# Kernel optimization log

Measured on AMD Instinct MI355X. Metric: run time of the kernel, lower is better.

The kernel has to match this reference:

```python
import jax, jax.numpy as jnp
import numpy as np
import math

B, N, D = 8, 4096, 1024
H = 8          # num_heads
NC = 2         # n_classes


def setup_inputs() -> dict:
    key = jax.random.key(0)
    ks = jax.random.split(key, 12)
    s = 1.0 / math.sqrt(D)
    return {
        "inputs": jax.random.normal(ks[0], (B, N, D), jnp.float32),
        # enc: Linear(D, 1) + Sigmoid
        "W_enc": jax.random.normal(ks[1], (1, D), jnp.float32) * s,
        "b_enc": jnp.zeros((1,), jnp.float32),
        "cls_token": jax.random.normal(ks[2], (1, 1, D), jnp.float32) * s,
        # depthwise Conv2d(D, D, 3, padding=1, groups=D)
        "conv_w": jax.random.normal(ks[3], (D, 1, 3, 3), jnp.float32) * 0.1,
        "conv_b": jnp.zeros((D,), jnp.float32),
        # MAB projections (torch Linear weight layout [out, in])
        "Wq": jax.random.normal(ks[4], (D, D), jnp.float32) * s,
        "bq": jnp.zeros((D,), jnp.float32),
        "Wk": jax.random.normal(ks[5], (D, D), jnp.float32) * s,
        "bk": jnp.zeros((D,), jnp.float32),
        "Wv": jax.random.normal(ks[6], (D, D), jnp.float32) * s,
        "bv": jnp.zeros((D,), jnp.float32),
        "Wo": jax.random.normal(ks[7], (D, D), jnp.float32) * s,
        "bo": jnp.zeros((D,), jnp.float32),
        # final classifier Linear(D, NC)
        "Wfc": jax.random.normal(ks[8], (NC, D), jnp.float32) * s,
        "bfc": jnp.zeros((NC,), jnp.float32),
    }


def reference(inputs, W_enc, b_enc, cls_token, conv_w, conv_b,
              Wq, bq, Wk, bk, Wv, bv, Wo, bo, Wfc, bfc):
    b, n, d = inputs.shape
    # ---- recalib(option='max', k=1): top-1 instance per bag as query ----
    a1 = jax.nn.sigmoid(inputs @ W_enc.T + b_enc)[..., 0]            # [B, N]
    idx = jnp.argmax(a1, axis=1)                                      # [B]
    Q = jnp.take_along_axis(inputs, idx[:, None, None], axis=1)       # [B, 1, D]
    # ---- shift_feature ----
    inputs = jax.nn.relu(inputs - Q)
    # ---- pad to square grid, prepend cls token ----
    _H = int(np.ceil(np.sqrt(n)))
    add = _H * _H - n
    x = jnp.concatenate([inputs, inputs[:, :add, :]], axis=1)         # [B, _H*_H, D]
    cls = jnp.broadcast_to(cls_token, (b, 1, d))
    x = jnp.concatenate([cls, x], axis=1)                             # [B, S, D]
    cls_tok, feat = x[:, 0], x[:, 1:]
    # ---- depthwise conv residual on the 2D grid ----
    cnn = feat.transpose(0, 2, 1).reshape(b, d, _H, _H)               # [B, C, H, W]
    conv = jax.lax.conv_general_dilated(
        cnn, conv_w, window_strides=(1, 1), padding='SAME',
        dimension_numbers=('NCHW', 'OIHW', 'NCHW'),
        feature_group_count=d) + conv_b[None, :, None, None]
    cnn = conv + cnn
    xf = cnn.reshape(b, d, _H * _H).transpose(0, 2, 1)
    x = jnp.concatenate([cls_tok[:, None, :], xf], axis=1)            # [B, S, D]
    # ---- MAB(Q, x): manual multi-head attention ----
    Qp = Q @ Wq.T + bq                                                # [B, 1, D]
    K = x @ Wk.T + bk                                                 # [B, S, D]
    V = x @ Wv.T + bv
    dh = d // H
    qh = Qp.reshape(b, 1, H, dh).transpose(0, 2, 1, 3)                # [B, H, 1, dh]
    kh = K.reshape(b, -1, H, dh).transpose(0, 2, 1, 3)                # [B, H, S, dh]
    vh = V.reshape(b, -1, H, dh).transpose(0, 2, 1, 3)
    # NOTE: original scales by sqrt(dim_V), not sqrt(d_head)
    logits = jnp.einsum('bhqd,bhkd->bhqk', qh, kh) / jnp.asarray(math.sqrt(d), jnp.float32)
    A = jax.nn.softmax(logits, axis=-1)
    oh = qh + jnp.einsum('bhqk,bhkd->bhqd', A, vh)                    # residual inside heads
    O = oh.transpose(0, 2, 1, 3).reshape(b, 1, d)                     # [B, 1, D]
    O = O + jax.nn.relu(O @ Wo.T + bo)
    bag = O[:, 0]                                                     # [B, D]
    out = bag @ Wfc.T + bfc                                           # [B, NC]
    return out
```

## Files before the change

### kernel.cpp

```cpp
#include <hip/hip_runtime.h>
#include <hip/hip_bf16.h>


#define NTOK 4096
#define DD 1024

#define FO_ARG 0
#define FO_CWT 4160
#define FO_QP  13376
#define FO_W   21568
#define FO_MS  87232
#define FO_YP  95424
#define FO_Y   4289728
#define FO_O1  4355264
#define FO_O2  4363456
#define FO_XF  8388608
#define FO_PL  41943040

#define LSTRIDE 101

__global__ void k_init(const float* __restrict__ convw, float* __restrict__ cwT,
                       unsigned long long* __restrict__ argbest) {
  int gid = blockIdx.x * 256 + threadIdx.x;
  if (gid < 8) argbest[gid] = 0ull;
  if (gid < 9216) {
    int d = gid / 9, p = gid - d * 9;
    cwT[p * DD + d] = convw[gid];
  }
}

__global__ void k_argmax1(const float* __restrict__ inp, const float* __restrict__ Wenc,
                          const float* __restrict__ benc, unsigned long long* __restrict__ argbest) {
  __shared__ unsigned long long lb[4];
  int wave = threadIdx.x >> 6, lane = threadIdx.x & 63;
  int b = blockIdx.x >> 8;
  int r0 = ((blockIdx.x & 255) << 4) + (wave << 2);
  const float4* base = (const float4*)(inp + ((size_t)b * NTOK + r0) * DD);
  const float4* wp = (const float4*)Wenc;
  float s0 = 0.f, s1 = 0.f, s2 = 0.f, s3 = 0.f;
#pragma unroll
  for (int k = 0; k < 4; ++k) {
    int off = lane + (k << 6);
    float4 w4 = wp[off];
    float4 a0 = base[off];
    float4 a1 = base[256 + off];
    float4 a2 = base[512 + off];
    float4 a3 = base[768 + off];
    s0 = fmaf(w4.x, a0.x, s0); s0 = fmaf(w4.y, a0.y, s0); s0 = fmaf(w4.z, a0.z, s0); s0 = fmaf(w4.w, a0.w, s0);
    s1 = fmaf(w4.x, a1.x, s1); s1 = fmaf(w4.y, a1.y, s1); s1 = fmaf(w4.z, a1.z, s1); s1 = fmaf(w4.w, a1.w, s1);
    s2 = fmaf(w4.x, a2.x, s2); s2 = fmaf(w4.y, a2.y, s2); s2 = fmaf(w4.z, a2.z, s2); s2 = fmaf(w4.w, a2.w, s2);
    s3 = fmaf(w4.x, a3.x, s3); s3 = fmaf(w4.y, a3.y, s3); s3 = fmaf(w4.z, a3.z, s3); s3 = fmaf(w4.w, a3.w, s3);
  }
#pragma unroll
  for (int mk = 32; mk >= 1; mk >>= 1) {
    s0 += __shfl_xor(s0, mk); s1 += __shfl_xor(s1, mk);
    s2 += __shfl_xor(s2, mk); s3 += __shfl_xor(s3, mk);
  }
  if (lane == 0) {
    float be = benc[0];
    float v[4] = {s0 + be, s1 + be, s2 + be, s3 + be};
    unsigned long long bst = 0ull;
#pragma unroll
    for (int i = 0; i < 4; ++i) {
      unsigned u = __float_as_uint(v[i]);
      u = (u & 0x80000000u) ? ~u : (u | 0x80000000u);
      unsigned long long p = ((unsigned long long)u << 32) |
                             (unsigned long long)(0xFFFFFFFFu - (unsigned)(r0 + i));
      bst = bst > p ? bst : p;
    }
    lb[wave] = bst;
  }
  __syncthreads();
  if (threadIdx.x == 0) {
    unsigned long long m = lb[0];
#pragma unroll
    for (int i = 1; i < 4; ++i) m = m > lb[i] ? m : lb[i];
    atomicMax(&argbest[b], m);
  }
}

__global__ void k_qp(const float* __restrict__ inp, const float* __restrict__ Wq,
                     const float* __restrict__ bq, const unsigned long long* __restrict__ argbest,
                     float* __restrict__ Qp) {
  int wave = threadIdx.x >> 6, lane = threadIdx.x & 63;
  int b = blockIdx.x >> 8;
  int i = ((blockIdx.x & 255) << 2) + wave;
  unsigned idx = 0xFFFFFFFFu - (unsigned)(argbest[b] & 0xFFFFFFFFull);
  const float4* qr = (const float4*)(inp + ((size_t)b * NTOK + idx) * DD);
  const float4* wr = (const float4*)(Wq + (size_t)i * DD);
  float s = 0.f;
#pragma unroll
  for (int k = 0; k < 4; ++k) {
    float4 a = wr[lane + (k << 6)], x = qr[lane + (k << 6)];
    s = fmaf(a.x, x.x, s); s = fmaf(a.y, x.y, s);
    s = fmaf(a.z, x.z, s); s = fmaf(a.w, x.w, s);
  }
  for (int m = 32; m > 0; m >>= 1) s += __shfl_xor(s, m);
  if (lane == 0) Qp[b * DD + i] = s + bq[i];
}

__global__ void k_w(const float* __restrict__ Wk, const float* __restrict__ Qp,
                    float* __restrict__ wbuf) {
  __shared__ float qs[1024];
  __shared__ float sred[2048];
  const int tid = threadIdx.x;
  const int h = blockIdx.x >> 5, jb = blockIdx.x & 31;
  {
    int b = tid >> 5, i4 = tid & 31;
    ((float4*)qs)[b * 32 + i4] = ((const float4*)Qp)[b * 256 + (h << 5) + i4];
  }
  __syncthreads();
  const int jl = tid & 31, ig = tid >> 5;
  const float* wkp = Wk + (size_t)((h << 7) + (ig << 4)) * DD + (jb << 5) + jl;
  float acc[8];
#pragma unroll
  for (int b = 0; b < 8; ++b) acc[b] = 0.f;
#pragma unroll
  for (int ii = 0; ii < 16; ++ii) {
    float wv = wkp[(size_t)ii * DD];
    int i = (ig << 4) + ii;
#pragma unroll
    for (int b = 0; b < 8; ++b) acc[b] = fmaf(qs[(b << 7) + i], wv, acc[b]);
  }
#pragma unroll
  for (int b = 0; b < 8; ++b) sred[ig * 256 + (b << 5) + jl] = acc[b];
  __syncthreads();
  {
    int b = tid >> 5, j2 = tid & 31;
    float s = 0.f;
#pragma unroll
    for (int g = 0; g < 8; ++g) s += sred[g * 256 + (b << 5) + j2];
    wbuf[(size_t)((b << 3) + h) * DD + (jb << 5) + j2] = s;
  }
}

__global__ __launch_bounds__(512, 4) void k_logits(
    const float* __restrict__ inp, const float* __restrict__ convb,
    const float* __restrict__ cwT, const float* __restrict__ wbuf,
    const unsigned long long* __restrict__ argbest,
    float* __restrict__ plog, float* __restrict__ xf) {
  __shared__ float4 sred4[2048];
  const int tid = threadIdx.x, bx = blockIdx.x;
  const int b = bx >> 10, tile = (bx >> 4) & 63, cidx = bx & 15;
  const int R0 = (tile >> 3) << 3, C0 = (tile & 7) << 3;
  const unsigned idxq = 0xFFFFFFFFu - (unsigned)(argbest[b] & 0xFFFFFFFFull);
  const float* inpb = inp + (size_t)b * NTOK * DD;
  const float* qrow = inpb + (size_t)idxq * DD;
  const int gg = tid & 15, ts = tid >> 4;
  const int jg = tid >> 5, rq = (tid >> 3) & 3, ca = tid & 7;
  const int r0a = rq << 1;
  const int jc = cidx << 6;

  float acc[2][8];
#pragma unroll
  for (int i = 0; i < 2; ++i)
#pragma unroll
    for (int h = 0; h < 8; ++h) acc[i][h] = 0.f;
  float4 xs0, xs1;

  {
    const int js = jc + (gg << 2);
    float4 qv = *(const float4*)(qrow + js);
    for (int t = ts; t < 100; t += 32) {
      int tr = t / 10, tc = t - tr * 10;
      int gr = R0 - 1 + tr, gc = C0 - 1 + tc;
      float4 v = make_float4(0.f, 0.f, 0.f, 0.f);
      if (gr >= 0 && gr < 64 && gc >= 0 && gc < 64) {
        float4 rv = *(const float4*)(inpb + (size_t)((gr << 6) + gc) * DD + js);
        v.x = fmaxf(rv.x - qv.x, 0.f); v.y = fmaxf(rv.y - qv.y, 0.f);
        v.z = fmaxf(rv.z - qv.z, 0.f); v.w = fmaxf(rv.w - qv.w, 0.f);
      }
      sred4[gg * LSTRIDE + t] = v;
    }
  }
  __syncthreads();
  {
    const int j4 = jc + (jg << 2);
    float4 cwr[9];
#pragma unroll
    for (int p = 0; p < 9; ++p) cwr[p] = *(const float4*)(cwT + p * DD + j4);
    float4 cb4 = *(const float4*)(convb + j4);
    const float4* fb = sred4 + jg * LSTRIDE;
    float4 x0 = cb4, x1 = cb4;
    {
      float4 rw[4][3];
#pragma unroll
      for (int rr = 0; rr < 4; ++rr)
#pragma unroll
        for (int dc = 0; dc < 3; ++dc)
          rw[rr][dc] = fb[(r0a + rr) * 10 + ca + dc];
#pragma unroll
      for (int dr = 0; dr < 3; ++dr)
#pragma unroll
        for (int dc = 0; dc < 3; ++dc) {
          float4 w = cwr[dr * 3 + dc];
          float4 f0 = rw[dr][dc], f1 = rw[dr + 1][dc];
          x0.x = fmaf(w.x, f0.x, x0.x); x0.y = fmaf(w.y, f0.y, x0.y);
          x0.z = fmaf(w.z, f0.z, x0.z); x0.w = fmaf(w.w, f0.w, x0.w);
          x1.x = fmaf(w.x, f1.x, x1.x); x1.y = fmaf(w.y, f1.y, x1.y);
          x1.z = fmaf(w.z, f1.z, x1.z); x1.w = fmaf(w.w, f1.w, x1.w);
        }
      x0.x += rw[1][1].x; x0.y += rw[1][1].y; x0.z += rw[1][1].z; x0.w += rw[1][1].w;
      x1.x += rw[2][1].x; x1.y += rw[2][1].y; x1.z += rw[2][1].z; x1.w += rw[2][1].w;
    }
    xs0 = x0; xs1 = x1;
#pragma unroll
    for (int h = 0; h < 8; ++h) {
      float4 whv = *(const float4*)(wbuf + (size_t)(b * 8 + h) * DD + j4);
      float a0 = acc[0][h], a1 = acc[1][h];
      a0 = fmaf(whv.x, x0.x, a0); a0 = fmaf(whv.y, x0.y, a0);
      a0 = fmaf(whv.z, x0.z, a0); a0 = fmaf(whv.w, x0.w, a0);
      a1 = fmaf(whv.x, x1.x, a1); a1 = fmaf(whv.y, x1.y, a1);
      a1 = fmaf(whv.z, x1.z, a1); a1 = fmaf(whv.w, x1.w, a1);
      acc[0][h] = a0; acc[1][h] = a1;
    }
  }
  __syncthreads();
  float* red = (float*)sred4;
#pragma unroll
  for (int it = 0; it < 2; ++it)
#pragma unroll
    for (int h = 0; h < 8; ++h)
      red[jg * 512 + ((r0a + it) * 8 + ca) * 8 + h] = acc[it][h];
  __syncthreads();
  {
    float s = 0.f;
#pragma unroll
    for (int g = 0; g < 16; ++g) s += red[g * 512 + tid];
    plog[(size_t)bx * 512 + tid] = s;
  }
  __syncthreads();
  float4* ldsx = sred4;
  {
    const int tk0 = (r0a << 3) + ca;
    ldsx[tk0 * 17 + jg] = xs0;
    ldsx[(tk0 + 8) * 17 + jg] = xs1;
  }
  __syncthreads();
  {
    float* xfb = xf + (size_t)((b << 6) + tile) * (64 * DD) + jc;
#pragma unroll
    for (int it = 0; it < 2; ++it) {
      int idx = (it << 9) + tid;
      int tk = idx >> 4, q = idx & 15;
      float4 v = ldsx[tk * 17 + q];
      *(float4*)(xfb + (size_t)tk * DD + (q << 2)) = v;
    }
  }
}

__global__ __launch_bounds__(512, 8) void k_ysum(
    const float* __restrict__ plog, const float* __restrict__ xf,
    float2* __restrict__ msbuf, float* __restrict__ ypart) {
  __shared__ float atile[512];
  const int tid = threadIdx.x, bt = blockIdx.x;
  {
    const float* pp = plog + (size_t)bt * 16 * 512;
    float s = 0.f;
#pragma unroll
    for (int c = 0; c < 16; ++c) s += pp[c * 512 + tid];
    atile[tid] = s * 0.03125f;
  }
  __syncthreads();
  {
    const int w = tid >> 6, l = tid & 63;
    float v = atile[l * 8 + w];
    float mx = v;
#pragma unroll
    for (int mk = 32; mk >= 1; mk >>= 1) mx = fmaxf(mx, __shfl_xor(mx, mk));
    float e = __expf(v - mx);
    float Ss = e;
#pragma unroll
    for (int mk = 32; mk >= 1; mk >>= 1) Ss += __shfl_xor(Ss, mk);
    __syncthreads();
    atile[l * 8 + w] = e;
    if (l == 0) {
      int b = bt >> 6, tile = bt & 63;
      msbuf[((b << 3) + w) * 64 + tile] = make_float2(mx, Ss);
    }
  }
  __syncthreads();
  const float* xbase = xf + (size_t)bt * (64 * DD) + (tid << 1);
  float2 acc[8];
#pragma unroll
  for (int h = 0; h < 8; ++h) acc[h] = make_float2(0.f, 0.f);
#pragma unroll 4
  for (int t = 0; t < 64; ++t) {
    float2 v = *(const float2*)(xbase + (size_t)t * DD);
    float4 aA = *(const float4*)&atile[t * 8];
    float4 aB = *(const float4*)&atile[t * 8 + 4];
    acc[0].x = fmaf(aA.x, v.x, acc[0].x); acc[0].y = fmaf(aA.x, v.y, acc[0].y);
    acc[1].x = fmaf(aA.y, v.x, acc[1].x); acc[1].y = fmaf(aA.y, v.y, acc[1].y);
    acc[2].x = fmaf(aA.z, v.x, acc[2].x); acc[2].y = fmaf(aA.z, v.y, acc[2].y);
    acc[3].x = fmaf(aA.w, v.x, acc[3].x); acc[3].y = fmaf(aA.w, v.y, acc[3].y);
    acc[4].x = fmaf(aB.x, v.x, acc[4].x); acc[4].y = fmaf(aB.x, v.y, acc[4].y);
    acc[5].x = fmaf(aB.y, v.x, acc[5].x); acc[5].y = fmaf(aB.y, v.y, acc[5].y);
    acc[6].x = fmaf(aB.z, v.x, acc[6].x); acc[6].y = fmaf(aB.z, v.y, acc[6].y);
    acc[7].x = fmaf(aB.w, v.x, acc[7].x); acc[7].y = fmaf(aB.w, v.y, acc[7].y);
  }
  const int b = bt >> 6, tile = bt & 63;
#pragma unroll
  for (int h = 0; h < 8; ++h)
    *(float2*)(ypart + ((size_t)((b * 8 + h) * 64 + tile)) * DD + (tid << 1)) = acc[h];
}

__global__ void k_comb(const float2* __restrict__ msbuf, const float* __restrict__ wbuf,
                       const float* __restrict__ cls, const float* __restrict__ ypart,
                       float* __restrict__ ybuf) {
  __shared__ float redl[256];
  __shared__ float wgt[64];
  __shared__ float wclss;
  __shared__ float4 sacc[256];
  int tid = threadIdx.x;
  int bh = blockIdx.x >> 3, cs = blockIdx.x & 7;
  {
    float4 a = ((const float4*)(wbuf + (size_t)bh * DD))[tid];
    float4 c = ((const float4*)cls)[tid];
    redl[tid] = a.x * c.x + a.y * c.y + a.z * c.z + a.w * c.w;
  }
  __syncthreads();
  for (int s = 128; s > 0; s >>= 1) { if (tid < s) redl[tid] += redl[tid + s]; __syncthreads(); }
  float l0 = redl[0] * 0.03125f;
  if (tid < 64) {
    float2 ms = msbuf[bh * 64 + tid];
    float m = ms.x, S = ms.y;
    float M = m;
#pragma unroll
    for (int mk = 32; mk >= 1; mk >>= 1) M = fmaxf(M, __shfl_xor(M, mk));
    M = fmaxf(M, l0);
    float w = __expf(m - M);
    float z = S * w;
#pragma unroll
    for (int mk = 32; mk >= 1; mk >>= 1) z += __shfl_xor(z, mk);
    float ec = __expf(l0 - M);
    float Z = z + ec;
    wgt[tid] = w / Z;
    if (tid == 0) wclss = ec / Z;
  }
  __syncthreads();
  int ch4 = (cs << 5) + (tid & 31);
  int tg = tid >> 5;
  const float* yp = ypart + (size_t)bh * 64 * DD + (ch4 << 2);
  float4 acc = make_float4(0.f, 0.f, 0.f, 0.f);
#pragma unroll
  for (int tt = 0; tt < 8; ++tt) {
    int t = tg * 8 + tt;
    float w = wgt[t];
    float4 v = *(const float4*)(yp + (size_t)t * DD);
    acc.x = fmaf(w, v.x, acc.x); acc.y = fmaf(w, v.y, acc.y);
    acc.z = fmaf(w, v.z, acc.z); acc.w = fmaf(w, v.w, acc.w);
  }
  sacc[tg * 32 + (tid & 31)] = acc;
  __syncthreads();
  if (tid < 32) {
    int c4 = (cs << 5) + tid;
    float4 s = sacc[tid];
#pragma unroll
    for (int g = 1; g < 8; ++g) {
      float4 v = sacc[g * 32 + tid];
      s.x += v.x; s.y += v.y; s.z += v.z; s.w += v.w;
    }
    float wc = wclss;
    float4 cv = *(const float4*)(cls + (c4 << 2));
    s.x = fmaf(wc, cv.x, s.x); s.y = fmaf(wc, cv.y, s.y);
    s.z = fmaf(wc, cv.z, s.z); s.w = fmaf(wc, cv.w, s.w);
    *(float4*)(ybuf + (size_t)bh * DD + (c4 << 2)) = s;
  }
}

__global__ void k_o1(const float* __restrict__ Wv, const float* __restrict__ bv,
                     const float* __restrict__ Qp, const float* __restrict__ ybuf,
                     float* __restrict__ O1) {
  int wave = threadIdx.x >> 6, lane = threadIdx.x & 63;
  int b = blockIdx.x >> 8;
  int i = ((blockIdx.x & 255) << 2) + wave;
  int h = i >> 7;
  const float4* wr = (const float4*)(Wv + (size_t)i * DD);
  const float4* yr = (const float4*)(ybuf + (size_t)(b * 8 + h) * DD);
  float s = 0.f;
#pragma unroll
  for (int k = 0; k < 4; ++k) {
    float4 a = wr[lane + (k << 6)], x = yr[lane + (k << 6)];
    s = fmaf(a.x, x.x, s); s = fmaf(a.y, x.y, s);
    s = fmaf(a.z, x.z, s); s = fmaf(a.w, x.w, s);
  }
  for (int m = 32; m > 0; m >>= 1) s += __shfl_xor(s, m);
  if (lane == 0) O1[b * DD + i] = Qp[b * DD + i] + bv[i] + s;
}

__global__ void k_o2(const float* __restrict__ Wo, const float* __restrict__ bo,
                     const float* __restrict__ O1, float* __restrict__ O2) {
  int wave = threadIdx.x >> 6, lane = threadIdx.x & 63;
  int b = blockIdx.x >> 8;
  int i = ((blockIdx.x & 255) << 2) + wave;
  const float4* wr = (const float4*)(Wo + (size_t)i * DD);
  const float4* xr = (const float4*)(O1 + (size_t)b * DD);
  float s = 0.f;
#pragma unroll
  for (int k = 0; k < 4; ++k) {
    float4 a = wr[lane + (k << 6)], x = xr[lane + (k << 6)];
    s = fmaf(a.x, x.x, s); s = fmaf(a.y, x.y, s);
    s = fmaf(a.z, x.z, s); s = fmaf(a.w, x.w, s);
  }
  for (int m = 32; m > 0; m >>= 1) s += __shfl_xor(s, m);
  if (lane == 0) O2[b * DD + i] = O1[b * DD + i] + fmaxf(s + bo[i], 0.f);
}

__global__ void k_out(const float* __restrict__ Wfc, const float* __restrict__ bfc,
                      const float* __restrict__ O2, float* __restrict__ out) {
  int wave = threadIdx.x >> 6, lane = threadIdx.x & 63;
  for (int p = wave; p < 16; p += 4) {
    int b = p >> 1, cc = p & 1;
    const float4* o = (const float4*)(O2 + (size_t)b * DD);
    const float4* wr = (const float4*)(Wfc + (size_t)cc * DD);
    float s = 0.f;
#pragma unroll
    for (int k = 0; k < 4; ++k) {
      float4 a = o[lane + (k << 6)], x = wr[lane + (k << 6)];
      s = fmaf(a.x, x.x, s); s = fmaf(a.y, x.y, s);
      s = fmaf(a.z, x.z, s); s = fmaf(a.w, x.w, s);
    }
    for (int m = 32; m > 0; m >>= 1) s += __shfl_xor(s, m);
    if (lane == 0) out[p] = s + bfc[cc];
  }
}

extern "C" void kernel_launch(void* const* d_in, const int* in_sizes, int n_in,
                              void* d_out, int out_size, void* d_ws, size_t ws_size,
                              hipStream_t stream) {
  const float* inp   = (const float*)d_in[0];
  const float* Wenc  = (const float*)d_in[1];
  const float* benc  = (const float*)d_in[2];
  const float* cls   = (const float*)d_in[3];
  const float* convw = (const float*)d_in[4];
  const float* convb = (const float*)d_in[5];
  const float* Wq    = (const float*)d_in[6];
  const float* bq    = (const float*)d_in[7];
  const float* Wk    = (const float*)d_in[8];
  const float* bv    = (const float*)d_in[11];
  const float* Wv    = (const float*)d_in[10];
  const float* Wo    = (const float*)d_in[12];
  const float* bo    = (const float*)d_in[13];
  const float* Wfc   = (const float*)d_in[14];
  const float* bfc   = (const float*)d_in[15];
  float* out = (float*)d_out;
  float* W = (float*)d_ws;
  unsigned long long* argbest = (unsigned long long*)(W + FO_ARG);
  float* cwT   = W + FO_CWT;
  float* Qp    = W + FO_QP;
  float* wbuf  = W + FO_W;
  float2* msbuf = (float2*)(W + FO_MS);
  float* ypart = W + FO_YP;
  float* plog  = W + FO_PL;
  float* xf    = W + FO_XF;
  float* ybuf  = W + FO_Y;
  float* O1    = W + FO_O1;
  float* O2    = W + FO_O2;

  hipLaunchKernelGGL(k_init,    dim3(36),   dim3(256), 0, stream, convw, cwT, argbest);
  hipLaunchKernelGGL(k_argmax1, dim3(2048), dim3(256), 0, stream, inp, Wenc, benc, argbest);
  hipLaunchKernelGGL(k_qp,      dim3(2048), dim3(256), 0, stream, inp, Wq, bq, argbest, Qp);
  hipLaunchKernelGGL(k_w,       dim3(256),  dim3(256), 0, stream, Wk, Qp, wbuf);
  hipLaunchKernelGGL(k_logits,  dim3(8192), dim3(512), 0, stream, inp, convb, cwT, wbuf, argbest, plog, xf);
  hipLaunchKernelGGL(k_ysum,    dim3(512),  dim3(512), 0, stream, plog, xf, msbuf, ypart);
  hipLaunchKernelGGL(k_comb,    dim3(512),  dim3(256), 0, stream, msbuf, wbuf, cls, ypart, ybuf);
  hipLaunchKernelGGL(k_o1,      dim3(2048), dim3(256), 0, stream, Wv, bv, Qp, ybuf, O1);
  hipLaunchKernelGGL(k_o2,      dim3(2048), dim3(256), 0, stream, Wo, bo, O1, O2);
  hipLaunchKernelGGL(k_out,     dim3(1),    dim3(256), 0, stream, Wfc, bfc, O2, out);
}
```

Baseline: 339.8 us.

## Fuse conv/logits and softmax-weighted sum into one kernel keeping features in registers

Merges k_logits and k_ysum into k_fuse. Each block now handles a whole 8x8 tile across all 1024 channels, looping over 16 channel chunks and holding the conv outputs in registers (32 float4). This removes the global round trip of xf and plog, about 128MB of writes and reads. The cost is only 512 blocks with heavy register pressure, launch bounds cut to 2 per SIMD, possible spills, and cross-lane shuffle reductions for the weighted sums.

After: 488.8 us. 1.44x slower.

```diff
diff --git a/kernel.cpp b/kernel.cpp
--- a/kernel.cpp
+++ b/kernel.cpp
@@ -14,8 +14,6 @@
 #define FO_Y   4289728
 #define FO_O1  4355264
 #define FO_O2  4363456
-#define FO_XF  8388608
-#define FO_PL  41943040
 
 #define LSTRIDE 101
 
@@ -134,14 +132,15 @@
   }
 }
 
-__global__ __launch_bounds__(512, 4) void k_logits(
+__global__ __launch_bounds__(512, 2) void k_fuse(
     const float* __restrict__ inp, const float* __restrict__ convb,
     const float* __restrict__ cwT, const float* __restrict__ wbuf,
     const unsigned long long* __restrict__ argbest,
-    float* __restrict__ plog, float* __restrict__ xf) {
+    float2* __restrict__ msbuf, float* __restrict__ ypart) {
   __shared__ float4 sred4[2048];
+  __shared__ float atile[512];
   const int tid = threadIdx.x, bx = blockIdx.x;
-  const int b = bx >> 10, tile = (bx >> 4) & 63, cidx = bx & 15;
+  const int b = bx >> 6, tile = bx & 63;
   const int R0 = (tile >> 3) << 3, C0 = (tile & 7) << 3;
   const unsigned idxq = 0xFFFFFFFFu - (unsigned)(argbest[b] & 0xFFFFFFFFull);
   const float* inpb = inp + (size_t)b * NTOK * DD;
@@ -149,70 +148,75 @@
   const int gg = tid & 15, ts = tid >> 4;
   const int jg = tid >> 5, rq = (tid >> 3) & 3, ca = tid & 7;
   const int r0a = rq << 1;
-  const int jc = cidx << 6;
+  const int tk0 = (r0a << 3) + ca;
 
   float acc[2][8];
 #pragma unroll
   for (int i = 0; i < 2; ++i)
 #pragma unroll
     for (int h = 0; h < 8; ++h) acc[i][h] = 0.f;
-  float4 xs0, xs1;
-
-  {
-    const int js = jc + (gg << 2);
-    float4 qv = *(const float4*)(qrow + js);
-    for (int t = ts; t < 100; t += 32) {
-      int tr = t / 10, tc = t - tr * 10;
-      int gr = R0 - 1 + tr, gc = C0 - 1 + tc;
-      float4 v = make_float4(0.f, 0.f, 0.f, 0.f);
-      if (gr >= 0 && gr < 64 && gc >= 0 && gc < 64) {
-        float4 rv = *(const float4*)(inpb + (size_t)((gr << 6) + gc) * DD + js);
-        v.x = fmaxf(rv.x - qv.x, 0.f); v.y = fmaxf(rv.y - qv.y, 0.f);
-        v.z = fmaxf(rv.z - qv.z, 0.f); v.w = fmaxf(rv.w - qv.w, 0.f);
+  float4 xsA[16], xsB[16];
+
+#pragma unroll
+  for (int cidx = 0; cidx < 16; ++cidx) {
+    const int jc = cidx << 6;
+    if (cidx) __syncthreads();
+    {
+      const int js = jc + (gg << 2);
+      float4 qv = *(const float4*)(qrow + js);
+      for (int t = ts; t < 100; t += 32) {
+        int tr = t / 10, tc = t - tr * 10;
+        int gr = R0 - 1 + tr, gc = C0 - 1 + tc;
+        float4 v = make_float4(0.f, 0.f, 0.f, 0.f);
+        if (gr >= 0 && gr < 64 && gc >= 0 && gc < 64) {
+          float4 rv = *(const float4*)(inpb + (size_t)((gr << 6) + gc) * DD + js);
+          v.x = fmaxf(rv.x - qv.x, 0.f); v.y = fmaxf(rv.y - qv.y, 0.f);
+          v.z = fmaxf(rv.z - qv.z, 0.f); v.w = fmaxf(rv.w - qv.w, 0.f);
+        }
+        sred4[gg * LSTRIDE + t] = v;
       }
-      sred4[gg * LSTRIDE + t] = v;
-    }
-  }
-  __syncthreads();
-  {
-    const int j4 = jc + (jg << 2);
-    float4 cwr[9];
-#pragma unroll
-    for (int p = 0; p < 9; ++p) cwr[p] = *(const float4*)(cwT + p * DD + j4);
-    float4 cb4 = *(const float4*)(convb + j4);
-    const float4* fb = sred4 + jg * LSTRIDE;
-    float4 x0 = cb4, x1 = cb4;
+    }
+    __syncthreads();
     {
-      float4 rw[4][3];
-#pragma unroll
-      for (int rr = 0; rr < 4; ++rr)
-#pragma unroll
-        for (int dc = 0; dc < 3; ++dc)
-          rw[rr][dc] = fb[(r0a + rr) * 10 + ca + dc];
-#pragma unroll
-      for (int dr = 0; dr < 3; ++dr)
-#pragma unroll
-        for (int dc = 0; dc < 3; ++dc) {
-          float4 w = cwr[dr * 3 + dc];
-          float4 f0 = rw[dr][dc], f1 = rw[dr + 1][dc];
-          x0.x = fmaf(w.x, f0.x, x0.x); x0.y = fmaf(w.y, f0.y, x0.y);
-          x0.z = fmaf(w.z, f0.z, x0.z); x0.w = fmaf(w.w, f0.w, x0.w);
-          x1.x = fmaf(w.x, f1.x, x1.x); x1.y = fmaf(w.y, f1.y, x1.y);
-          x1.z = fmaf(w.z, f1.z, x1.z); x1.w = fmaf(w.w, f1.w, x1.w);
-        }
-      x0.x += rw[1][1].x; x0.y += rw[1][1].y; x0.z += rw[1][1].z; x0.w += rw[1][1].w;
-      x1.x += rw[2][1].x; x1.y += rw[2][1].y; x1.z += rw[2][1].z; x1.w += rw[2][1].w;
-    }
-    xs0 = x0; xs1 = x1;
-#pragma unroll
-    for (int h = 0; h < 8; ++h) {
-      float4 whv = *(const float4*)(wbuf + (size_t)(b * 8 + h) * DD + j4);
-      float a0 = acc[0][h], a1 = acc[1][h];
-      a0 = fmaf(whv.x, x0.x, a0); a0 = fmaf(whv.y, x0.y, a0);
-      a0 = fmaf(whv.z, x0.z, a0); a0 = fmaf(whv.w, x0.w, a0);
-      a1 = fmaf(whv.x, x1.x, a1); a1 = fmaf(whv.y, x1.y, a1);
-      a1 = fmaf(whv.z, x1.z, a1); a1 = fmaf(whv.w, x1.w, a1);
-      acc[0][h] = a0; acc[1][h] = a1;
+      const int j4 = jc + (jg << 2);
+      float4 cwr[9];
+#pragma unroll
+      for (int p = 0; p < 9; ++p) cwr[p] = *(const float4*)(cwT + p * DD + j4);
+      float4 cb4 = *(const float4*)(convb + j4);
+      const float4* fb = sred4 + jg * LSTRIDE;
+      float4 x0 = cb4, x1 = cb4;
+      {
+        float4 rw[4][3];
+#pragma unroll
+        for (int rr = 0; rr < 4; ++rr)
+#pragma unroll
+          for (int dc = 0; dc < 3; ++dc)
+            rw[rr][dc] = fb[(r0a + rr) * 10 + ca + dc];
+#pragma unroll
+        for (int dr = 0; dr < 3; ++dr)
+#pragma unroll
+          for (int dc = 0; dc < 3; ++dc) {
+            float4 w = cwr[dr * 3 + dc];
+            float4 f0 = rw[dr][dc], f1 = rw[dr + 1][dc];
+            x0.x = fmaf(w.x, f0.x, x0.x); x0.y = fmaf(w.y, f0.y, x0.y);
+            x0.z = fmaf(w.z, f0.z, x0.z); x0.w = fmaf(w.w, f0.w, x0.w);
+            x1.x = fmaf(w.x, f1.x, x1.x); x1.y = fmaf(w.y, f1.y, x1.y);
+            x1.z = fmaf(w.z, f1.z, x1.z); x1.w = fmaf(w.w, f1.w, x1.w);
+          }
+        x0.x += rw[1][1].x; x0.y += rw[1][1].y; x0.z += rw[1][1].z; x0.w += rw[1][1].w;
+        x1.x += rw[2][1].x; x1.y += rw[2][1].y; x1.z += rw[2][1].z; x1.w += rw[2][1].w;
+      }
+      xsA[cidx] = x0; xsB[cidx] = x1;
+#pragma unroll
+      for (int h = 0; h < 8; ++h) {
+        float4 whv = *(const float4*)(wbuf + (size_t)(b * 8 + h) * DD + j4);
+        float a0 = acc[0][h], a1 = acc[1][h];
+        a0 = fmaf(whv.x, x0.x, a0); a0 = fmaf(whv.y, x0.y, a0);
+        a0 = fmaf(whv.z, x0.z, a0); a0 = fmaf(whv.w, x0.w, a0);
+        a1 = fmaf(whv.x, x1.x, a1); a1 = fmaf(whv.y, x1.y, a1);
+        a1 = fmaf(whv.z, x1.z, a1); a1 = fmaf(whv.w, x1.w, a1);
+        acc[0][h] = a0; acc[1][h] = a1;
+      }
     }
   }
   __syncthreads();
@@ -227,38 +231,6 @@
     float s = 0.f;
 #pragma unroll
     for (int g = 0; g < 16; ++g) s += red[g * 512 + tid];
-    plog[(size_t)bx * 512 + tid] = s;
-  }
-  __syncthreads();
-  float4* ldsx = sred4;
-  {
-    const int tk0 = (r0a << 3) + ca;
-    ldsx[tk0 * 17 + jg] = xs0;
-    ldsx[(tk0 + 8) * 17 + jg] = xs1;
-  }
-  __syncthreads();
-  {
-    float* xfb = xf + (size_t)((b << 6) + tile) * (64 * DD) + jc;
-#pragma unroll
-    for (int it = 0; it < 2; ++it) {
-      int idx = (it << 9) + tid;
-      int tk = idx >> 4, q = idx & 15;
-      float4 v = ldsx[tk * 17 + q];
-      *(float4*)(xfb + (size_t)tk * DD + (q << 2)) = v;
-    }
-  }
-}
-
-__global__ __launch_bounds__(512, 8) void k_ysum(
-    const float* __restrict__ plog, const float* __restrict__ xf,
-    float2* __restrict__ msbuf, float* __restrict__ ypart) {
-  __shared__ float atile[512];
-  const int tid = threadIdx.x, bt = blockIdx.x;
-  {
-    const float* pp = plog + (size_t)bt * 16 * 512;
-    float s = 0.f;
-#pragma unroll
-    for (int c = 0; c < 16; ++c) s += pp[c * 512 + tid];
     atile[tid] = s * 0.03125f;
   }
   __syncthreads();
@@ -274,34 +246,57 @@
     for (int mk = 32; mk >= 1; mk >>= 1) Ss += __shfl_xor(Ss, mk);
     __syncthreads();
     atile[l * 8 + w] = e;
-    if (l == 0) {
-      int b = bt >> 6, tile = bt & 63;
-      msbuf[((b << 3) + w) * 64 + tile] = make_float2(mx, Ss);
-    }
-  }
-  __syncthreads();
-  const float* xbase = xf + (size_t)bt * (64 * DD) + (tid << 1);
-  float2 acc[8];
-#pragma unroll
-  for (int h = 0; h < 8; ++h) acc[h] = make_float2(0.f, 0.f);
-#pragma unroll 4
-  for (int t = 0; t < 64; ++t) {
-    float2 v = *(const float2*)(xbase + (size_t)t * DD);
-    float4 aA = *(const float4*)&atile[t * 8];
-    float4 aB = *(const float4*)&atile[t * 8 + 4];
-    acc[0].x = fmaf(aA.x, v.x, acc[0].x); acc[0].y = fmaf(aA.x, v.y, acc[0].y);
-    acc[1].x = fmaf(aA.y, v.x, acc[1].x); acc[1].y = fmaf(aA.y, v.y, acc[1].y);
-    acc[2].x = fmaf(aA.z, v.x, acc[2].x); acc[2].y = fmaf(aA.z, v.y, acc[2].y);
-    acc[3].x = fmaf(aA.w, v.x, acc[3].x); acc[3].y = fmaf(aA.w, v.y, acc[3].y);
-    acc[4].x = fmaf(aB.x, v.x, acc[4].x); acc[4].y = fmaf(aB.x, v.y, acc[4].y);
-    acc[5].x = fmaf(aB.y, v.x, acc[5].x); acc[5].y = fmaf(aB.y, v.y, acc[5].y);
-    acc[6].x = fmaf(aB.z, v.x, acc[6].x); acc[6].y = fmaf(aB.z, v.y, acc[6].y);
-    acc[7].x = fmaf(aB.w, v.x, acc[7].x); acc[7].y = fmaf(aB.w, v.y, acc[7].y);
-  }
-  const int b = bt >> 6, tile = bt & 63;
-#pragma unroll
-  for (int h = 0; h < 8; ++h)
-    *(float2*)(ypart + ((size_t)((b * 8 + h) * 64 + tile)) * DD + (tid << 1)) = acc[h];
+    if (l == 0) msbuf[((b << 3) + w) * 64 + tile] = make_float2(mx, Ss);
+  }
+  __syncthreads();
+  float* yout = (float*)sred4;
+  const float4 aA = *(const float4*)&atile[tk0 * 8];
+  const float4 aB = *(const float4*)&atile[tk0 * 8 + 4];
+  const float4 cA = *(const float4*)&atile[(tk0 + 8) * 8];
+  const float4 cB = *(const float4*)&atile[(tk0 + 8) * 8 + 4];
+#pragma unroll
+  for (int cidx = 0; cidx < 16; ++cidx) {
+    float4 x0 = xsA[cidx], x1 = xsB[cidx];
+    float4 y[8];
+    y[0].x = fmaf(aA.x, x0.x, cA.x * x1.x); y[0].y = fmaf(aA.x, x0.y, cA.x * x1.y);
+    y[0].z = fmaf(aA.x, x0.z, cA.x * x1.z); y[0].w = fmaf(aA.x, x0.w, cA.x * x1.w);
+    y[1].x = fmaf(aA.y, x0.x, cA.y * x1.x); y[1].y = fmaf(aA.y, x0.y, cA.y * x1.y);
+    y[1].z = fmaf(aA.y, x0.z, cA.y * x1.z); y[1].w = fmaf(aA.y, x0.w, cA.y * x1.w);
+    y[2].x = fmaf(aA.z, x0.x, cA.z * x1.x); y[2].y = fmaf(aA.z, x0.y, cA.z * x1.y);
+    y[2].z = fmaf(aA.z, x0.z, cA.z * x1.z); y[2].w = fmaf(aA.z, x0.w, cA.z * x1.w);
+    y[3].x = fmaf(aA.w, x0.x, cA.w * x1.x); y[3].y = fmaf(aA.w, x0.y, cA.w * x1.y);
+    y[3].z = fmaf(aA.w, x0.z, cA.w * x1.z); y[3].w = fmaf(aA.w, x0.w, cA.w * x1.w);
+    y[4].x = fmaf(aB.x, x0.x, cB.x * x1.x); y[4].y = fmaf(aB.x, x0.y, cB.x * x1.y);
+    y[4].z = fmaf(aB.x, x0.z, cB.x * x1.z); y[4].w = fmaf(aB.x, x0.w, cB.x * x1.w);
+    y[5].x = fmaf(aB.y, x0.x, cB.y * x1.x); y[5].y = fmaf(aB.y, x0.y, cB.y * x1.y);
+    y[5].z = fmaf(aB.y, x0.z, cB.y * x1.z); y[5].w = fmaf(aB.y, x0.w, cB.y * x1.w);
+    y[6].x = fmaf(aB.z, x0.x, cB.z * x1.x); y[6].y = fmaf(aB.z, x0.y, cB.z * x1.y);
+    y[6].z = fmaf(aB.z, x0.z, cB.z * x1.z); y[6].w = fmaf(aB.z, x0.w, cB.z * x1.w);
+    y[7].x = fmaf(aB.w, x0.x, cB.w * x1.x); y[7].y = fmaf(aB.w, x0.y, cB.w * x1.y);
+    y[7].z = fmaf(aB.w, x0.z, cB.w * x1.z); y[7].w = fmaf(aB.w, x0.w, cB.w * x1.w);
+#pragma unroll
+    for (int mk = 16; mk >= 1; mk >>= 1)
+#pragma unroll
+      for (int h = 0; h < 8; ++h) {
+        y[h].x += __shfl_xor(y[h].x, mk);
+        y[h].y += __shfl_xor(y[h].y, mk);
+        y[h].z += __shfl_xor(y[h].z, mk);
+        y[h].w += __shfl_xor(y[h].w, mk);
+      }
+    if ((tid & 31) == 0) {
+#pragma unroll
+      for (int h = 0; h < 8; ++h)
+        ((float4*)yout)[h * 256 + (cidx << 4) + jg] = y[h];
+    }
+  }
+  __syncthreads();
+#pragma unroll
+  for (int it = 0; it < 4; ++it) {
+    int idx = (it << 9) + tid;
+    int h = idx >> 8, q = idx & 255;
+    *(float4*)(ypart + ((size_t)((b * 8 + h) * 64 + tile)) * DD + (q << 2)) =
+        ((const float4*)yout)[idx];
+  }
 }
 
 __global__ void k_comb(const float2* __restrict__ msbuf, const float* __restrict__ wbuf,
@@ -451,8 +446,6 @@
   float* wbuf  = W + FO_W;
   float2* msbuf = (float2*)(W + FO_MS);
   float* ypart = W + FO_YP;
-  float* plog  = W + FO_PL;
-  float* xf    = W + FO_XF;
   float* ybuf  = W + FO_Y;
   float* O1    = W + FO_O1;
   float* O2    = W + FO_O2;
@@ -461,8 +454,7 @@
   hipLaunchKernelGGL(k_argmax1, dim3(2048), dim3(256), 0, stream, inp, Wenc, benc, argbest);
   hipLaunchKernelGGL(k_qp,      dim3(2048), dim3(256), 0, stream, inp, Wq, bq, argbest, Qp);
   hipLaunchKernelGGL(k_w,       dim3(256),  dim3(256), 0, stream, Wk, Qp, wbuf);
-  hipLaunchKernelGGL(k_logits,  dim3(8192), dim3(512), 0, stream, inp, convb, cwT, wbuf, argbest, plog, xf);
-  hipLaunchKernelGGL(k_ysum,    dim3(512),  dim3(512), 0, stream, plog, xf, msbuf, ypart);
+  hipLaunchKernelGGL(k_fuse,    dim3(512),  dim3(512), 0, stream, inp, convb, cwT, wbuf, argbest, msbuf, ypart);
   hipLaunchKernelGGL(k_comb,    dim3(512),  dim3(256), 0, stream, msbuf, wbuf, cls, ypart, ybuf);
   hipLaunchKernelGGL(k_o1,      dim3(2048), dim3(256), 0, stream, Wv, bv, Qp, ybuf, O1);
   hipLaunchKernelGGL(k_o2,      dim3(2048), dim3(256), 0, stream, Wo, bo, O1, O2);
```
